# Optimization experiments

Hardware: AMD Instinct MI355X
Metric: run time of the kernel (lower is better)

## Reference

```python
import jax, jax.numpy as jnp
import numpy as np

N_HEAD = 16
EPS = 1e-6


def setup_inputs() -> dict:
    key = jax.random.key(0)
    ks = jax.random.split(key, 5)
    B, T, C = 2, 2048, 1024
    hd = C // N_HEAD
    x = jax.random.normal(ks[0], (B, T, C), dtype=jnp.float32)
    # rotary frequencies (unit-magnitude complex, decomposed into cos/sin)
    theta = 10000.0 ** (-np.arange(0, hd, 2, dtype=np.float32) / hd)  # [hd/2]
    ang = np.arange(T, dtype=np.float32)[:, None] * theta[None, :]    # [T, hd/2]
    freqs_cos = jnp.asarray(np.cos(ang))
    freqs_sin = jnp.asarray(np.sin(ang))
    w_attn = jax.random.normal(ks[1], (3 * C, C), dtype=jnp.float32) * 0.02
    w_proj = jax.random.normal(ks[2], (C, C), dtype=jnp.float32) * 0.02
    q_norm_w = jnp.ones((hd,), dtype=jnp.float32)
    k_norm_w = jnp.ones((hd,), dtype=jnp.float32)
    return {"x": x, "freqs_cos": freqs_cos, "freqs_sin": freqs_sin,
            "w_attn": w_attn, "w_proj": w_proj,
            "q_norm_w": q_norm_w, "k_norm_w": k_norm_w}


def _rmsnorm(x, w):
    # x: [..., hd]; per-last-dim RMSNorm with learned scale
    rms = jax.lax.rsqrt(jnp.mean(x * x, axis=-1, keepdims=True) + EPS)
    return x * rms * w


def _rope(x, cos, sin):
    # x: [B, T, H, hd]; cos/sin: [T, hd/2] -> broadcast [1, T, 1, hd/2]
    x2 = x.reshape(*x.shape[:-1], -1, 2)  # [B,T,H,hd/2,2]
    x0, x1 = x2[..., 0], x2[..., 1]
    c = cos[None, :, None, :]
    s = sin[None, :, None, :]
    r0 = x0 * c - x1 * s
    r1 = x0 * s + x1 * c
    return jnp.stack([r0, r1], axis=-1).reshape(x.shape)


def reference(x, freqs_cos, freqs_sin, w_attn, w_proj, q_norm_w, k_norm_w):
    B, T, C = x.shape
    H = N_HEAD
    hd = C // H
    qkv = x @ w_attn.T  # [B, T, 3C]
    q, k, v = jnp.split(qkv, 3, axis=-1)
    q = q.reshape(B, T, H, hd)
    k = k.reshape(B, T, H, hd)
    v = v.reshape(B, T, H, hd)
    q = _rmsnorm(q, q_norm_w)
    k = _rmsnorm(k, k_norm_w)
    q = _rope(q, freqs_cos[:T], freqs_sin[:T])
    k = _rope(k, freqs_cos[:T], freqs_sin[:T])
    scale = 1.0 / jnp.sqrt(jnp.asarray(hd, dtype=x.dtype))
    # causal SDPA: scores [B, H, T, T]
    scores = jnp.einsum('bihd,bjhd->bhij', q, k) * scale
    causal = jnp.tril(jnp.ones((T, T), dtype=bool))
    scores = jnp.where(causal[None, None], scores, jnp.finfo(scores.dtype).min)
    p = jax.nn.softmax(scores, axis=-1)
    y = jnp.einsum('bhij,bjhd->bihd', p, v).reshape(B, T, C)
    return y @ w_proj.T
```

## Files before the change

kernel.cpp:

```cpp
#include <hip/hip_runtime.h>

typedef unsigned short u16;
typedef unsigned int u32;
typedef __bf16 bf16x8 __attribute__((ext_vector_type(8)));
typedef float f32x4 __attribute__((ext_vector_type(4)));

__device__ __forceinline__ u16 f2bf(float f) {
    union { float f; u32 u; } v;
    v.f = f;
    u32 r = v.u + 0x7fffu + ((v.u >> 16) & 1u);
    return (u16)(r >> 16);
}

__device__ __forceinline__ u32 fbits(float f) {
    union { float f; u32 u; } v; v.f = f; return v.u;
}

__device__ __forceinline__ void glds16(const void* g, void* l) {
    __builtin_amdgcn_global_load_lds(
        (__attribute__((address_space(1))) unsigned int*)(g),
        (__attribute__((address_space(3))) unsigned int*)(l), 16, 0, 0);
}

__global__ void castbf3(const float* __restrict__ a, u16* __restrict__ oa,
                        const float* __restrict__ b, u16* __restrict__ ob,
                        const float* __restrict__ c, u16* __restrict__ oc) {
    int blk = blockIdx.x;
    if (blk < 4096) {
        int i = blk * 256 + threadIdx.x;
        float4 v = ((const float4*)a)[i];
        ushort4 o;
        o.x = f2bf(v.x); o.y = f2bf(v.y); o.z = f2bf(v.z); o.w = f2bf(v.w);
        ((ushort4*)oa)[i] = o;
    } else if (blk < 7168) {
        int i = (blk - 4096) * 256 + threadIdx.x;
        int n = i >> 8, c4 = i & 255;
        int np;
        if (n < 2048) {
            int part = n >> 10, rem = n & 1023;
            int h = rem >> 6, d = rem & 63;
            int nd = (d >> 1) + ((d & 1) << 5);
            np = part * 1024 + h * 64 + nd;
        } else np = n;
        float4 v = ((const float4*)b)[i];
        ushort4 o;
        o.x = f2bf(v.x); o.y = f2bf(v.y); o.z = f2bf(v.z); o.w = f2bf(v.w);
        ((ushort4*)ob)[np * 256 + c4] = o;
    } else {
        int i = (blk - 7168) * 256 + threadIdx.x;
        float4 v = ((const float4*)c)[i];
        ushort4 o;
        o.x = f2bf(v.x); o.y = f2bf(v.y); o.z = f2bf(v.z); o.w = f2bf(v.w);
        ((ushort4*)oc)[i] = o;
    }
}

__global__ __launch_bounds__(256) void gemm_qkv(
    const u16* __restrict__ A, const u16* __restrict__ B,
    const float* __restrict__ fcos, const float* __restrict__ fsin,
    const float* __restrict__ qw, const float* __restrict__ kw,
    u16* __restrict__ q, u16* __restrict__ k, u16* __restrict__ vt)
{
    __shared__ alignas(16) u16 As[128 * 32];
    __shared__ alignas(16) u16 Bs[128 * 32];
    __shared__ alignas(16) u16 Es[2 * 128 * 64];
    const int tid = threadIdx.x;
    const int lane = tid & 63;
    const int wave = tid >> 6;
    const int bm = blockIdx.y * 128, bn = blockIdx.x * 128;
    const int wm = (wave >> 1) * 64, wn = (wave & 1) * 64;
    const int ln = lane & 15, quad = lane >> 4;
    const int K = 1024;

    f32x4 acc[4][4] = {};

    const int srow = tid >> 2;
    const int scol = (tid & 3) * 8;
    const u16* gA = A + (size_t)(bm + srow) * K + scol;
    const u16* gB = B + (size_t)(bn + srow) * K + scol;
    u16* lA = &As[wave * 512];
    u16* lB = &Bs[wave * 512];

    for (int k0 = 0; k0 < K; k0 += 32) {
        glds16(gA + k0, lA);
        glds16(gA + (size_t)64 * K + k0, lA + 2048);
        glds16(gB + k0, lB);
        glds16(gB + (size_t)64 * K + k0, lB + 2048);
        __builtin_amdgcn_s_waitcnt(0);
        __syncthreads();

        bf16x8 af[4], bfr[4];
#pragma unroll
        for (int i = 0; i < 4; ++i)
            af[i] = *(const bf16x8*)&As[(wm + i * 16 + ln) * 32 + quad * 8];
#pragma unroll
        for (int j = 0; j < 4; ++j)
            bfr[j] = *(const bf16x8*)&Bs[(wn + j * 16 + ln) * 32 + quad * 8];
#pragma unroll
        for (int i = 0; i < 4; ++i)
#pragma unroll
            for (int j = 0; j < 4; ++j)
                acc[i][j] = __builtin_amdgcn_mfma_f32_16x16x32_bf16(af[i], bfr[j], acc[i][j], 0, 0, 0);
        __syncthreads();
    }

    const int part = bn >> 10;
    const int headw = wave & 1;
    const int h0 = (bn & 1023) >> 6;
    const float SC = 0.18033688011112042f;

    if (part == 2) {
#pragma unroll
        for (int i = 0; i < 4; ++i)
#pragma unroll
            for (int r = 0; r < 4; ++r) {
                int tloc = wm + i * 16 + quad * 4 + r;
#pragma unroll
                for (int j = 0; j < 4; ++j) {
                    int d = j * 16 + ln;
                    Es[headw * 8192 + d * 128 + (tloc ^ (ln << 3))] = f2bf(acc[i][j][r]);
                }
            }
        __syncthreads();
        const int b = bm >> 11, tbase = bm & 2047;
#pragma unroll
        for (int c = 0; c < 8; ++c) {
            int cid = c * 256 + tid;
            int tc = cid & 15, d = (cid >> 4) & 63, hd = cid >> 10;
            uint4 v = *(const uint4*)&Es[hd * 8192 + d * 128 + ((tc ^ (d & 15)) << 3)];
            size_t dst = ((size_t)((b * 16 + h0 + hd) * 64 + d)) * 2048
                       + tbase + ((tc >> 3) << 6) + (((tc & 7) ^ (d & 7)) << 3);
            *(uint4*)&vt[dst] = v;
        }
        return;
    }

    const float* nw = (part == 0) ? qw : kw;
    float wv[4];
#pragma unroll
    for (int j = 0; j < 4; ++j) {
        int nd = j * 16 + ln;
        int od = ((nd & 31) << 1) | (nd >> 5);
        wv[j] = nw[od];
    }

#pragma unroll
    for (int i = 0; i < 4; ++i) {
#pragma unroll
        for (int r = 0; r < 4; ++r) {
            int tloc = wm + i * 16 + quad * 4 + r;
            int t = (bm + tloc) & 2047;

            float v0 = acc[i][0][r], v1 = acc[i][1][r];
            float v2 = acc[i][2][r], v3 = acc[i][3][r];
            float ss = v0 * v0 + v1 * v1 + v2 * v2 + v3 * v3;
            ss += __shfl_xor(ss, 1);
            ss += __shfl_xor(ss, 2);
            ss += __shfl_xor(ss, 4);
            ss += __shfl_xor(ss, 8);
            float g = rsqrtf(ss * (1.0f / 64.0f) + 1e-6f);
            if (part == 0) g *= SC;

            float x0a = v0 * g * wv[0], x0b = v1 * g * wv[1];
            float x1a = v2 * g * wv[2], x1b = v3 * g * wv[3];
            float c0 = fcos[t * 32 + ln],      s0 = fsin[t * 32 + ln];
            float c1 = fcos[t * 32 + 16 + ln], s1 = fsin[t * 32 + 16 + ln];
            float o0 = x0a * c0 - x1a * s0;
            float o2 = x0a * s0 + x1a * c0;
            float o1 = x0b * c1 - x1b * s1;
            float o3 = x0b * s1 + x1b * c1;

            u16* e = &Es[headw * 8192 + tloc * 64 + ln];
            e[((0 ^ quad) << 4)] = f2bf(o0);
            e[((1 ^ quad) << 4)] = f2bf(o1);
            e[((2 ^ quad) << 4)] = f2bf(o2);
            e[((3 ^ quad) << 4)] = f2bf(o3);
        }
    }
    __syncthreads();
#pragma unroll
    for (int c = 0; c < 8; ++c) {
        int cid = c * 256 + tid;
        int dc = cid & 7, tloc = (cid >> 3) & 127, hd = cid >> 10;
        int q2 = (tloc >> 2) & 3;
        int sq = (dc >> 1) ^ q2;
        uint4 v = *(const uint4*)&Es[hd * 8192 + tloc * 64 + sq * 16 + (dc & 1) * 8];
        int gm = bm + tloc;
        int b = gm >> 11, t = gm & 2047;
        size_t rb = ((size_t)((b * 16 + h0 + hd) * 2048 + t)) * 64;
        if (part == 0) *(uint4*)&q[rb + dc * 8] = v;
        else           *(uint4*)&k[rb + ((dc ^ (t & 7)) << 3)] = v;
    }
}

__global__ __launch_bounds__(256) void gemm64(
    const u16* __restrict__ A, const u16* __restrict__ B,
    float* __restrict__ C, int M, int N, int K)
{
    __shared__ alignas(16) u16 As[64 * 32];
    __shared__ alignas(16) u16 Bs[128 * 32];
    const int tid = threadIdx.x;
    const int lane = tid & 63;
    const int wave = tid >> 6;
    const int bm = blockIdx.y * 64, bn = blockIdx.x * 128;
    const int wm = (wave >> 1) * 32, wn = (wave & 1) * 64;
    const int ln = lane & 15, quad = lane >> 4;

    f32x4 acc[2][4] = {};

    const int srow = tid >> 2;
    const int scol = (tid & 3) * 8;
    const u16* gA = A + (size_t)(bm + (srow & 63)) * K + scol;
    const u16* gB = B + (size_t)(bn + srow) * K + scol;
    u16* lA = &As[wave * 512];
    u16* lB = &Bs[wave * 512];

    for (int k0 = 0; k0 < K; k0 += 32) {
        glds16(gA + k0, lA);
        glds16(gB + k0, lB);
        glds16(gB + (size_t)64 * K + k0, lB + 2048);
        __builtin_amdgcn_s_waitcnt(0);
        __syncthreads();

        bf16x8 af[2], bfr[4];
#pragma unroll
        for (int i = 0; i < 2; ++i)
            af[i] = *(const bf16x8*)&As[(wm + i * 16 + ln) * 32 + quad * 8];
#pragma unroll
        for (int j = 0; j < 4; ++j)
            bfr[j] = *(const bf16x8*)&Bs[(wn + j * 16 + ln) * 32 + quad * 8];
#pragma unroll
        for (int i = 0; i < 2; ++i)
#pragma unroll
            for (int j = 0; j < 4; ++j)
                acc[i][j] = __builtin_amdgcn_mfma_f32_16x16x32_bf16(af[i], bfr[j], acc[i][j], 0, 0, 0);
        __syncthreads();
    }

#pragma unroll
    for (int i = 0; i < 2; ++i) {
#pragma unroll
        for (int r = 0; r < 4; ++r) {
            int gm = bm + wm + i * 16 + quad * 4 + r;
            float* Crow = C + (size_t)gm * N + bn + wn + ln;
#pragma unroll
            for (int j = 0; j < 4; ++j)
                Crow[j * 16] = acc[i][j][r];
        }
    }
}

__global__ __launch_bounds__(256) void attn_kernel(
    const u16* __restrict__ Q, const u16* __restrict__ K,
    const u16* __restrict__ VT, u16* __restrict__ Y)
{
    __shared__ alignas(16) u16 Ks[2][64 * 64];
    __shared__ alignas(16) u16 Vs[2][64 * 64];
    __shared__ alignas(16) u16 Ps[4][16 * 80];

    const int tid = threadIdx.x;
    const int lane = tid & 63;
    const int wave = tid >> 6;
    const int ln = lane & 15, quad = lane >> 4;
    const int pi = blockIdx.x;
    const int bh = blockIdx.y;
    const int qaIdx = pi, qbIdx = 31 - pi;
    const int qA = qaIdx * 64, qB = qbIdx * 64;
    const size_t base = (size_t)bh * 2048 * 64;
    const u16* Kg = K + base;
    const u16* Vg = VT + base;

    const int qrowA = qA + wave * 16 + ln;
    bf16x8 qfA0 = *(const bf16x8*)&Q[base + (size_t)qrowA * 64 + quad * 8];
    bf16x8 qfA1 = *(const bf16x8*)&Q[base + (size_t)qrowA * 64 + 32 + quad * 8];
    const int qrowB = qB + wave * 16 + ln;
    bf16x8 qfB0 = *(const bf16x8*)&Q[base + (size_t)qrowB * 64 + quad * 8];
    bf16x8 qfB1 = *(const bf16x8*)&Q[base + (size_t)qrowB * 64 + 32 + quad * 8];

    f32x4 oA[4] = {}, oB[4] = {};
    float lA = 0.0f, lB = 0.0f;
    const int nstages = qbIdx + 1;
    const int sw = ln & 7;

    const int srow = wave * 16 + (lane >> 3);
    const int scol = (lane & 7) * 8;

    auto process = [&](const bf16x8& qf0, const bf16x8& qf1, float& l,
                       f32x4* o, const u16* ksb, const u16* vsb, bool domask,
                       int jb, int qb0) {
        f32x4 st[4];
#pragma unroll
        for (int ct = 0; ct < 4; ++ct) {
            bf16x8 kf0 = *(const bf16x8*)&ksb[(ct * 16 + ln) * 64 + ((0 + quad) ^ sw) * 8];
            bf16x8 kf1 = *(const bf16x8*)&ksb[(ct * 16 + ln) * 64 + ((4 + quad) ^ sw) * 8];
            f32x4 z = {};
            z = __builtin_amdgcn_mfma_f32_16x16x32_bf16(kf0, qf0, z, 0, 0, 0);
            st[ct] = __builtin_amdgcn_mfma_f32_16x16x32_bf16(kf1, qf1, z, 0, 0, 0);
        }
        if (domask) {
            const int qg = qb0 + wave * 16 + ln;
#pragma unroll
            for (int ct = 0; ct < 4; ++ct)
#pragma unroll
                for (int r = 0; r < 4; ++r) {
                    int kvg = jb + ct * 16 + quad * 4 + r;
                    if (kvg > qg) st[ct][r] = -1e30f;
                }
        }

        float sum = 0.0f;
#pragma unroll
        for (int ct = 0; ct < 4; ++ct) {
            float e0 = exp2f(st[ct][0]);
            float e1 = exp2f(st[ct][1]);
            float e2 = exp2f(st[ct][2]);
            float e3 = exp2f(st[ct][3]);
            sum += (e0 + e1) + (e2 + e3);
            uint2 pk;
            pk.x = __builtin_amdgcn_perm(fbits(e1), fbits(e0), 0x07060302u);
            pk.y = __builtin_amdgcn_perm(fbits(e3), fbits(e2), 0x07060302u);
            *(uint2*)&Ps[wave][ln * 80 + ct * 16 + quad * 4] = pk;
        }
        sum += __shfl_xor(sum, 16);
        sum += __shfl_xor(sum, 32);
        l += sum;

        __builtin_amdgcn_s_waitcnt(0xC07F);
        bf16x8 pf0 = *(const bf16x8*)&Ps[wave][ln * 80 + quad * 8];
        bf16x8 pf1 = *(const bf16x8*)&Ps[wave][ln * 80 + 32 + quad * 8];

#pragma unroll
        for (int dt = 0; dt < 4; ++dt) {
            bf16x8 vf0 = *(const bf16x8*)&vsb[(dt * 16 + ln) * 64 + ((0 + quad) ^ sw) * 8];
            bf16x8 vf1 = *(const bf16x8*)&vsb[(dt * 16 + ln) * 64 + ((4 + quad) ^ sw) * 8];
            o[dt] = __builtin_amdgcn_mfma_f32_16x16x32_bf16(pf0, vf0, o[dt], 0, 0, 0);
            o[dt] = __builtin_amdgcn_mfma_f32_16x16x32_bf16(pf1, vf1, o[dt], 0, 0, 0);
        }
    };

    glds16(&Kg[(size_t)(0 + srow) * 64 + scol],       &Ks[0][wave * 1024]);
    glds16(&Kg[(size_t)(0 + srow + 8) * 64 + scol],   &Ks[0][wave * 1024 + 512]);
    glds16(&Vg[(size_t)srow * 2048 + 0 + scol],       &Vs[0][wave * 1024]);
    glds16(&Vg[(size_t)(srow + 8) * 2048 + 0 + scol], &Vs[0][wave * 1024 + 512]);

    for (int jt = 0; jt < nstages; ++jt) {
        const int jb = jt * 64;
        const int jbn = (jt + 1 < nstages) ? (jt + 1) * 64 : 0;
        const int nb = (jt + 1) & 1;
        glds16(&Kg[(size_t)(jbn + srow) * 64 + scol],       &Ks[nb][wave * 1024]);
        glds16(&Kg[(size_t)(jbn + srow + 8) * 64 + scol],   &Ks[nb][wave * 1024 + 512]);
        glds16(&Vg[(size_t)srow * 2048 + jbn + scol],       &Vs[nb][wave * 1024]);
        glds16(&Vg[(size_t)(srow + 8) * 2048 + jbn + scol], &Vs[nb][wave * 1024 + 512]);

        asm volatile("s_waitcnt vmcnt(4)\n\ts_barrier" ::: "memory");

        const u16* ksb = &Ks[jt & 1][0];
        const u16* vsb = &Vs[jt & 1][0];

        if (jt <= qaIdx)
            process(qfA0, qfA1, lA, oA, ksb, vsb, jt == qaIdx, jb, qA);
        process(qfB0, qfB1, lB, oB, ksb, vsb, jt == qbIdx, jb, qB);

        asm volatile("s_waitcnt lgkmcnt(0)\n\ts_barrier" ::: "memory");
    }

    const int b = bh >> 4, h = bh & 15;
#pragma unroll
    for (int r = 0; r < 4; ++r) {
        float lra = __shfl(lA, (lane & 48) + quad * 4 + r);
        float invA = 1.0f / lra;
        int gqA = qA + wave * 16 + quad * 4 + r;
        size_t ybA = ((size_t)(b * 2048 + gqA)) * 1024 + h * 64 + ln;
        float lrb = __shfl(lB, (lane & 48) + quad * 4 + r);
        float invB = 1.0f / lrb;
        int gqB = qB + wave * 16 + quad * 4 + r;
        size_t ybB = ((size_t)(b * 2048 + gqB)) * 1024 + h * 64 + ln;
#pragma unroll
        for (int dt = 0; dt < 4; ++dt) {
            Y[ybA + dt * 16] = f2bf(oA[dt][r] * invA);
            Y[ybB + dt * 16] = f2bf(oB[dt][r] * invB);
        }
    }
}

extern "C" void kernel_launch(void* const* d_in, const int* in_sizes, int n_in,
                              void* d_out, int out_size, void* d_ws, size_t ws_size,
                              hipStream_t stream) {
    const float* x      = (const float*)d_in[0];
    const float* fcos   = (const float*)d_in[1];
    const float* fsin   = (const float*)d_in[2];
    const float* w_attn = (const float*)d_in[3];
    const float* w_proj = (const float*)d_in[4];
    const float* qw     = (const float*)d_in[5];
    const float* kw     = (const float*)d_in[6];
    float* out = (float*)d_out;

    char* ws = (char*)d_ws;
    u16* xb  = (u16*)(ws + 0);
    u16* wab = (u16*)(ws + 8388608);
    u16* wpb = (u16*)(ws + 14680064);
    u16* yb  = (u16*)(ws + 16777216);
    u16* qb  = (u16*)(ws + 25165824);
    u16* kb  = (u16*)(ws + 33554432);
    u16* vtb = (u16*)(ws + 41943040);

    castbf3<<<8192, 256, 0, stream>>>(x, xb, w_attn, wab, w_proj, wpb);

    gemm_qkv<<<dim3(24, 32), 256, 0, stream>>>(xb, wab, fcos, fsin, qw, kw, qb, kb, vtb);

    attn_kernel<<<dim3(16, 32), 256, 0, stream>>>(qb, kb, vtb, yb);

    gemm64<<<dim3(8, 64), 256, 0, stream>>>(yb, wpb, out, 4096, 1024, 1024);
}
```

Measured before the change: 212.2 us.

## Interleave paired query-tile attention stages and pack cos/sin and V stores

```diff
diff --git a/kernel.cpp b/kernel.cpp
--- a/kernel.cpp
+++ b/kernel.cpp
@@ -22,9 +22,13 @@
         (__attribute__((address_space(3))) unsigned int*)(l), 16, 0, 0);
 }
 
+#define MFMA __builtin_amdgcn_mfma_f32_16x16x32_bf16
+
 __global__ void castbf3(const float* __restrict__ a, u16* __restrict__ oa,
                         const float* __restrict__ b, u16* __restrict__ ob,
-                        const float* __restrict__ c, u16* __restrict__ oc) {
+                        const float* __restrict__ c, u16* __restrict__ oc,
+                        const float* __restrict__ fcos, const float* __restrict__ fsin,
+                        float2* __restrict__ csb) {
     int blk = blockIdx.x;
     if (blk < 4096) {
         int i = blk * 256 + threadIdx.x;
@@ -46,18 +50,21 @@
         ushort4 o;
         o.x = f2bf(v.x); o.y = f2bf(v.y); o.z = f2bf(v.z); o.w = f2bf(v.w);
         ((ushort4*)ob)[np * 256 + c4] = o;
-    } else {
+    } else if (blk < 8192) {
         int i = (blk - 7168) * 256 + threadIdx.x;
         float4 v = ((const float4*)c)[i];
         ushort4 o;
         o.x = f2bf(v.x); o.y = f2bf(v.y); o.z = f2bf(v.z); o.w = f2bf(v.w);
         ((ushort4*)oc)[i] = o;
+    } else {
+        int i = (blk - 8192) * 256 + threadIdx.x;
+        csb[i] = make_float2(fcos[i], fsin[i]);
     }
 }
 
 __global__ __launch_bounds__(256) void gemm_qkv(
     const u16* __restrict__ A, const u16* __restrict__ B,
-    const float* __restrict__ fcos, const float* __restrict__ fsin,
+    const float2* __restrict__ csb,
     const float* __restrict__ qw, const float* __restrict__ kw,
     u16* __restrict__ q, u16* __restrict__ k, u16* __restrict__ vt)
 {
@@ -100,7 +107,7 @@
         for (int i = 0; i < 4; ++i)
 #pragma unroll
             for (int j = 0; j < 4; ++j)
-                acc[i][j] = __builtin_amdgcn_mfma_f32_16x16x32_bf16(af[i], bfr[j], acc[i][j], 0, 0, 0);
+                acc[i][j] = MFMA(af[i], bfr[j], acc[i][j], 0, 0, 0);
         __syncthreads();
     }
 
@@ -111,16 +118,17 @@
 
     if (part == 2) {
 #pragma unroll
-        for (int i = 0; i < 4; ++i)
-#pragma unroll
-            for (int r = 0; r < 4; ++r) {
-                int tloc = wm + i * 16 + quad * 4 + r;
-#pragma unroll
-                for (int j = 0; j < 4; ++j) {
-                    int d = j * 16 + ln;
-                    Es[headw * 8192 + d * 128 + (tloc ^ (ln << 3))] = f2bf(acc[i][j][r]);
-                }
+        for (int i = 0; i < 4; ++i) {
+            int tlb = wm + i * 16 + quad * 4;
+#pragma unroll
+            for (int j = 0; j < 4; ++j) {
+                int d = j * 16 + ln;
+                uint2 pk;
+                pk.x = __builtin_amdgcn_perm(fbits(acc[i][j][1]), fbits(acc[i][j][0]), 0x07060302u);
+                pk.y = __builtin_amdgcn_perm(fbits(acc[i][j][3]), fbits(acc[i][j][2]), 0x07060302u);
+                *(uint2*)&Es[headw * 8192 + d * 128 + (tlb ^ (ln << 3))] = pk;
             }
+        }
         __syncthreads();
         const int b = bm >> 11, tbase = bm & 2047;
 #pragma unroll
@@ -163,12 +171,12 @@
 
             float x0a = v0 * g * wv[0], x0b = v1 * g * wv[1];
             float x1a = v2 * g * wv[2], x1b = v3 * g * wv[3];
-            float c0 = fcos[t * 32 + ln],      s0 = fsin[t * 32 + ln];
-            float c1 = fcos[t * 32 + 16 + ln], s1 = fsin[t * 32 + 16 + ln];
-            float o0 = x0a * c0 - x1a * s0;
-            float o2 = x0a * s0 + x1a * c0;
-            float o1 = x0b * c1 - x1b * s1;
-            float o3 = x0b * s1 + x1b * c1;
+            float2 cs0 = csb[t * 32 + ln];
+            float2 cs1 = csb[t * 32 + 16 + ln];
+            float o0 = x0a * cs0.x - x1a * cs0.y;
+            float o2 = x0a * cs0.y + x1a * cs0.x;
+            float o1 = x0b * cs1.x - x1b * cs1.y;
+            float o3 = x0b * cs1.y + x1b * cs1.x;
 
             u16* e = &Es[headw * 8192 + tloc * 64 + ln];
             e[((0 ^ quad) << 4)] = f2bf(o0);
@@ -233,7 +241,7 @@
         for (int i = 0; i < 2; ++i)
 #pragma unroll
             for (int j = 0; j < 4; ++j)
-                acc[i][j] = __builtin_amdgcn_mfma_f32_16x16x32_bf16(af[i], bfr[j], acc[i][j], 0, 0, 0);
+                acc[i][j] = MFMA(af[i], bfr[j], acc[i][j], 0, 0, 0);
         __syncthreads();
     }
 
@@ -246,6 +254,98 @@
 #pragma unroll
             for (int j = 0; j < 4; ++j)
                 Crow[j * 16] = acc[i][j][r];
+        }
+    }
+}
+
+template <bool DUAL>
+__device__ __forceinline__ void attn_stage(
+    int ln, int quad, int sw,
+    const u16* __restrict__ ksb, const u16* __restrict__ vsb,
+    u16* __restrict__ PsA, u16* __restrict__ PsB,
+    const bf16x8& qfA0, const bf16x8& qfA1,
+    const bf16x8& qfB0, const bf16x8& qfB1,
+    f32x4* oA, f32x4* oB, float& lA, float& lB,
+    bool maskA, bool maskB, int jb, int qA, int qB)
+{
+    f32x4 stA[4], stB[4];
+#pragma unroll
+    for (int ct = 0; ct < 4; ++ct) {
+        bf16x8 kf0 = *(const bf16x8*)&ksb[(ct * 16 + ln) * 64 + ((0 + quad) ^ sw) * 8];
+        bf16x8 kf1 = *(const bf16x8*)&ksb[(ct * 16 + ln) * 64 + ((4 + quad) ^ sw) * 8];
+        f32x4 z = {};
+        z = MFMA(kf0, qfB0, z, 0, 0, 0);
+        stB[ct] = MFMA(kf1, qfB1, z, 0, 0, 0);
+        if (DUAL) {
+            f32x4 za = {};
+            za = MFMA(kf0, qfA0, za, 0, 0, 0);
+            stA[ct] = MFMA(kf1, qfA1, za, 0, 0, 0);
+        }
+    }
+    if (maskB) {
+        const int qg = qB + ln;
+#pragma unroll
+        for (int ct = 0; ct < 4; ++ct)
+#pragma unroll
+            for (int r = 0; r < 4; ++r)
+                if (jb + ct * 16 + quad * 4 + r > qg) stB[ct][r] = -1e30f;
+    }
+    if (DUAL && maskA) {
+        const int qg = qA + ln;
+#pragma unroll
+        for (int ct = 0; ct < 4; ++ct)
+#pragma unroll
+            for (int r = 0; r < 4; ++r)
+                if (jb + ct * 16 + quad * 4 + r > qg) stA[ct][r] = -1e30f;
+    }
+
+    float sumB = 0.0f, sumA = 0.0f;
+#pragma unroll
+    for (int ct = 0; ct < 4; ++ct) {
+        float b0 = exp2f(stB[ct][0]), b1 = exp2f(stB[ct][1]);
+        float b2 = exp2f(stB[ct][2]), b3 = exp2f(stB[ct][3]);
+        sumB += (b0 + b1) + (b2 + b3);
+        uint2 pk;
+        pk.x = __builtin_amdgcn_perm(fbits(b1), fbits(b0), 0x07060302u);
+        pk.y = __builtin_amdgcn_perm(fbits(b3), fbits(b2), 0x07060302u);
+        *(uint2*)&PsB[ln * 80 + ct * 16 + quad * 4] = pk;
+        if (DUAL) {
+            float a0 = exp2f(stA[ct][0]), a1 = exp2f(stA[ct][1]);
+            float a2 = exp2f(stA[ct][2]), a3 = exp2f(stA[ct][3]);
+            sumA += (a0 + a1) + (a2 + a3);
+            uint2 pa;
+            pa.x = __builtin_amdgcn_perm(fbits(a1), fbits(a0), 0x07060302u);
+            pa.y = __builtin_amdgcn_perm(fbits(a3), fbits(a2), 0x07060302u);
+            *(uint2*)&PsA[ln * 80 + ct * 16 + quad * 4] = pa;
+        }
+    }
+    sumB += __shfl_xor(sumB, 16);
+    sumB += __shfl_xor(sumB, 32);
+    lB += sumB;
+    if (DUAL) {
+        sumA += __shfl_xor(sumA, 16);
+        sumA += __shfl_xor(sumA, 32);
+        lA += sumA;
+    }
+
+    __builtin_amdgcn_s_waitcnt(0xC07F);
+    bf16x8 pfB0 = *(const bf16x8*)&PsB[ln * 80 + quad * 8];
+    bf16x8 pfB1 = *(const bf16x8*)&PsB[ln * 80 + 32 + quad * 8];
+    bf16x8 pfA0, pfA1;
+    if (DUAL) {
+        pfA0 = *(const bf16x8*)&PsA[ln * 80 + quad * 8];
+        pfA1 = *(const bf16x8*)&PsA[ln * 80 + 32 + quad * 8];
+    }
+
+#pragma unroll
+    for (int dt = 0; dt < 4; ++dt) {
+        bf16x8 vf0 = *(const bf16x8*)&vsb[(dt * 16 + ln) * 64 + ((0 + quad) ^ sw) * 8];
+        bf16x8 vf1 = *(const bf16x8*)&vsb[(dt * 16 + ln) * 64 + ((4 + quad) ^ sw) * 8];
+        oB[dt] = MFMA(pfB0, vf0, oB[dt], 0, 0, 0);
+        oB[dt] = MFMA(pfB1, vf1, oB[dt], 0, 0, 0);
+        if (DUAL) {
+            oA[dt] = MFMA(pfA0, vf0, oA[dt], 0, 0, 0);
+            oA[dt] = MFMA(pfA1, vf1, oA[dt], 0, 0, 0);
         }
     }
 }
@@ -256,7 +356,8 @@
 {
     __shared__ alignas(16) u16 Ks[2][64 * 64];
     __shared__ alignas(16) u16 Vs[2][64 * 64];
-    __shared__ alignas(16) u16 Ps[4][16 * 80];
+    __shared__ alignas(16) u16 PsA[4][16 * 80];
+    __shared__ alignas(16) u16 PsB[4][16 * 80];
 
     const int tid = threadIdx.x;
     const int lane = tid & 63;
@@ -285,82 +386,34 @@
     const int srow = wave * 16 + (lane >> 3);
     const int scol = (lane & 7) * 8;
 
-    auto process = [&](const bf16x8& qf0, const bf16x8& qf1, float& l,
-                       f32x4* o, const u16* ksb, const u16* vsb, bool domask,
-                       int jb, int qb0) {
-        f32x4 st[4];
-#pragma unroll
-        for (int ct = 0; ct < 4; ++ct) {
-            bf16x8 kf0 = *(const bf16x8*)&ksb[(ct * 16 + ln) * 64 + ((0 + quad) ^ sw) * 8];
-            bf16x8 kf1 = *(const bf16x8*)&ksb[(ct * 16 + ln) * 64 + ((4 + quad) ^ sw) * 8];
-            f32x4 z = {};
-            z = __builtin_amdgcn_mfma_f32_16x16x32_bf16(kf0, qf0, z, 0, 0, 0);
-            st[ct] = __builtin_amdgcn_mfma_f32_16x16x32_bf16(kf1, qf1, z, 0, 0, 0);
-        }
-        if (domask) {
-            const int qg = qb0 + wave * 16 + ln;
-#pragma unroll
-            for (int ct = 0; ct < 4; ++ct)
-#pragma unroll
-                for (int r = 0; r < 4; ++r) {
-                    int kvg = jb + ct * 16 + quad * 4 + r;
-                    if (kvg > qg) st[ct][r] = -1e30f;
-                }
-        }
-
-        float sum = 0.0f;
-#pragma unroll
-        for (int ct = 0; ct < 4; ++ct) {
-            float e0 = exp2f(st[ct][0]);
-            float e1 = exp2f(st[ct][1]);
-            float e2 = exp2f(st[ct][2]);
-            float e3 = exp2f(st[ct][3]);
-            sum += (e0 + e1) + (e2 + e3);
-            uint2 pk;
-            pk.x = __builtin_amdgcn_perm(fbits(e1), fbits(e0), 0x07060302u);
-            pk.y = __builtin_amdgcn_perm(fbits(e3), fbits(e2), 0x07060302u);
-            *(uint2*)&Ps[wave][ln * 80 + ct * 16 + quad * 4] = pk;
-        }
-        sum += __shfl_xor(sum, 16);
-        sum += __shfl_xor(sum, 32);
-        l += sum;
-
-        __builtin_amdgcn_s_waitcnt(0xC07F);
-        bf16x8 pf0 = *(const bf16x8*)&Ps[wave][ln * 80 + quad * 8];
-        bf16x8 pf1 = *(const bf16x8*)&Ps[wave][ln * 80 + 32 + quad * 8];
-
-#pragma unroll
-        for (int dt = 0; dt < 4; ++dt) {
-            bf16x8 vf0 = *(const bf16x8*)&vsb[(dt * 16 + ln) * 64 + ((0 + quad) ^ sw) * 8];
-            bf16x8 vf1 = *(const bf16x8*)&vsb[(dt * 16 + ln) * 64 + ((4 + quad) ^ sw) * 8];
-            o[dt] = __builtin_amdgcn_mfma_f32_16x16x32_bf16(pf0, vf0, o[dt], 0, 0, 0);
-            o[dt] = __builtin_amdgcn_mfma_f32_16x16x32_bf16(pf1, vf1, o[dt], 0, 0, 0);
-        }
-    };
-
-    glds16(&Kg[(size_t)(0 + srow) * 64 + scol],       &Ks[0][wave * 1024]);
-    glds16(&Kg[(size_t)(0 + srow + 8) * 64 + scol],   &Ks[0][wave * 1024 + 512]);
-    glds16(&Vg[(size_t)srow * 2048 + 0 + scol],       &Vs[0][wave * 1024]);
-    glds16(&Vg[(size_t)(srow + 8) * 2048 + 0 + scol], &Vs[0][wave * 1024 + 512]);
-
-    for (int jt = 0; jt < nstages; ++jt) {
-        const int jb = jt * 64;
-        const int jbn = (jt + 1 < nstages) ? (jt + 1) * 64 : 0;
-        const int nb = (jt + 1) & 1;
+    auto prefetch = [&](int jbn, int nb) {
         glds16(&Kg[(size_t)(jbn + srow) * 64 + scol],       &Ks[nb][wave * 1024]);
         glds16(&Kg[(size_t)(jbn + srow + 8) * 64 + scol],   &Ks[nb][wave * 1024 + 512]);
         glds16(&Vg[(size_t)srow * 2048 + jbn + scol],       &Vs[nb][wave * 1024]);
         glds16(&Vg[(size_t)(srow + 8) * 2048 + jbn + scol], &Vs[nb][wave * 1024 + 512]);
-
+    };
+
+    prefetch(0, 0);
+
+    int jt = 0;
+    for (; jt <= qaIdx; ++jt) {
+        const int jbn = (jt + 1 < nstages) ? (jt + 1) * 64 : 0;
+        prefetch(jbn, (jt + 1) & 1);
         asm volatile("s_waitcnt vmcnt(4)\n\ts_barrier" ::: "memory");
-
-        const u16* ksb = &Ks[jt & 1][0];
-        const u16* vsb = &Vs[jt & 1][0];
-
-        if (jt <= qaIdx)
-            process(qfA0, qfA1, lA, oA, ksb, vsb, jt == qaIdx, jb, qA);
-        process(qfB0, qfB1, lB, oB, ksb, vsb, jt == qbIdx, jb, qB);
-
+        attn_stage<true>(ln, quad, sw, &Ks[jt & 1][0], &Vs[jt & 1][0],
+                         &PsA[wave][0], &PsB[wave][0],
+                         qfA0, qfA1, qfB0, qfB1, oA, oB, lA, lB,
+                         jt == qaIdx, false, jt * 64, qA + wave * 16, qB + wave * 16);
+        asm volatile("s_waitcnt lgkmcnt(0)\n\ts_barrier" ::: "memory");
+    }
+    for (; jt < nstages; ++jt) {
+        const int jbn = (jt + 1 < nstages) ? (jt + 1) * 64 : 0;
+        prefetch(jbn, (jt + 1) & 1);
+        asm volatile("s_waitcnt vmcnt(4)\n\ts_barrier" ::: "memory");
+        attn_stage<false>(ln, quad, sw, &Ks[jt & 1][0], &Vs[jt & 1][0],
+                          &PsA[wave][0], &PsB[wave][0],
+                          qfA0, qfA1, qfB0, qfB1, oA, oB, lA, lB,
+                          false, jt == qbIdx, jt * 64, qA + wave * 16, qB + wave * 16);
         asm volatile("s_waitcnt lgkmcnt(0)\n\ts_barrier" ::: "memory");
     }
 
@@ -396,17 +449,18 @@
     float* out = (float*)d_out;
 
     char* ws = (char*)d_ws;
-    u16* xb  = (u16*)(ws + 0);
-    u16* wab = (u16*)(ws + 8388608);
-    u16* wpb = (u16*)(ws + 14680064);
-    u16* yb  = (u16*)(ws + 16777216);
-    u16* qb  = (u16*)(ws + 25165824);
-    u16* kb  = (u16*)(ws + 33554432);
-    u16* vtb = (u16*)(ws + 41943040);
-
-    castbf3<<<8192, 256, 0, stream>>>(x, xb, w_attn, wab, w_proj, wpb);
-
-    gemm_qkv<<<dim3(24, 32), 256, 0, stream>>>(xb, wab, fcos, fsin, qw, kw, qb, kb, vtb);
+    u16*    xb  = (u16*)(ws + 0);
+    u16*    wab = (u16*)(ws + 8388608);
+    u16*    wpb = (u16*)(ws + 14680064);
+    u16*    yb  = (u16*)(ws + 16777216);
+    u16*    qb  = (u16*)(ws + 25165824);
+    u16*    kb  = (u16*)(ws + 33554432);
+    u16*    vtb = (u16*)(ws + 41943040);
+    float2* csb = (float2*)(ws + 50331648);
+
+    castbf3<<<8448, 256, 0, stream>>>(x, xb, w_attn, wab, w_proj, wpb, fcos, fsin, csb);
+
+    gemm_qkv<<<dim3(24, 32), 256, 0, stream>>>(xb, wab, csb, qw, kw, qb, kb, vtb);
 
     attn_kernel<<<dim3(16, 32), 256, 0, stream>>>(qb, kb, vtb, yb);
 
```

Measured after the change: 209.0 us. Within noise of the previous version (-1.5%).

## Split attention query pair across 8 waves and store Q transposed

Applied to the files above, without the earlier changes.

```diff
diff --git a/kernel.cpp b/kernel.cpp
--- a/kernel.cpp
+++ b/kernel.cpp
@@ -22,9 +22,13 @@
         (__attribute__((address_space(3))) unsigned int*)(l), 16, 0, 0);
 }
 
+#define MFMA __builtin_amdgcn_mfma_f32_16x16x32_bf16
+
 __global__ void castbf3(const float* __restrict__ a, u16* __restrict__ oa,
                         const float* __restrict__ b, u16* __restrict__ ob,
-                        const float* __restrict__ c, u16* __restrict__ oc) {
+                        const float* __restrict__ c, u16* __restrict__ oc,
+                        const float* __restrict__ fcos, const float* __restrict__ fsin,
+                        float2* __restrict__ csb) {
     int blk = blockIdx.x;
     if (blk < 4096) {
         int i = blk * 256 + threadIdx.x;
@@ -46,18 +50,21 @@
         ushort4 o;
         o.x = f2bf(v.x); o.y = f2bf(v.y); o.z = f2bf(v.z); o.w = f2bf(v.w);
         ((ushort4*)ob)[np * 256 + c4] = o;
-    } else {
+    } else if (blk < 8192) {
         int i = (blk - 7168) * 256 + threadIdx.x;
         float4 v = ((const float4*)c)[i];
         ushort4 o;
         o.x = f2bf(v.x); o.y = f2bf(v.y); o.z = f2bf(v.z); o.w = f2bf(v.w);
         ((ushort4*)oc)[i] = o;
+    } else {
+        int i = (blk - 8192) * 256 + threadIdx.x;
+        csb[i] = make_float2(fcos[i], fsin[i]);
     }
 }
 
 __global__ __launch_bounds__(256) void gemm_qkv(
     const u16* __restrict__ A, const u16* __restrict__ B,
-    const float* __restrict__ fcos, const float* __restrict__ fsin,
+    const float2* __restrict__ csb,
     const float* __restrict__ qw, const float* __restrict__ kw,
     u16* __restrict__ q, u16* __restrict__ k, u16* __restrict__ vt)
 {
@@ -100,7 +107,7 @@
         for (int i = 0; i < 4; ++i)
 #pragma unroll
             for (int j = 0; j < 4; ++j)
-                acc[i][j] = __builtin_amdgcn_mfma_f32_16x16x32_bf16(af[i], bfr[j], acc[i][j], 0, 0, 0);
+                acc[i][j] = MFMA(af[i], bfr[j], acc[i][j], 0, 0, 0);
         __syncthreads();
     }
 
@@ -108,21 +115,22 @@
     const int headw = wave & 1;
     const int h0 = (bn & 1023) >> 6;
     const float SC = 0.18033688011112042f;
+    const int b = bm >> 11, tbase = bm & 2047;
 
     if (part == 2) {
 #pragma unroll
-        for (int i = 0; i < 4; ++i)
-#pragma unroll
-            for (int r = 0; r < 4; ++r) {
-                int tloc = wm + i * 16 + quad * 4 + r;
-#pragma unroll
-                for (int j = 0; j < 4; ++j) {
-                    int d = j * 16 + ln;
-                    Es[headw * 8192 + d * 128 + (tloc ^ (ln << 3))] = f2bf(acc[i][j][r]);
-                }
-            }
-        __syncthreads();
-        const int b = bm >> 11, tbase = bm & 2047;
+        for (int i = 0; i < 4; ++i) {
+            int tlb = wm + i * 16 + quad * 4;
+#pragma unroll
+            for (int j = 0; j < 4; ++j) {
+                int d = j * 16 + ln;
+                uint2 pk;
+                pk.x = __builtin_amdgcn_perm(fbits(acc[i][j][1]), fbits(acc[i][j][0]), 0x07060302u);
+                pk.y = __builtin_amdgcn_perm(fbits(acc[i][j][3]), fbits(acc[i][j][2]), 0x07060302u);
+                *(uint2*)&Es[headw * 8192 + d * 128 + (tlb ^ (ln << 3))] = pk;
+            }
+        }
+        __syncthreads();
 #pragma unroll
         for (int c = 0; c < 8; ++c) {
             int cid = c * 256 + tid;
@@ -142,6 +150,52 @@
         int nd = j * 16 + ln;
         int od = ((nd & 31) << 1) | (nd >> 5);
         wv[j] = nw[od];
+    }
+
+    if (part == 0) {
+#pragma unroll
+        for (int i = 0; i < 4; ++i) {
+            float oj[4][4];
+#pragma unroll
+            for (int r = 0; r < 4; ++r) {
+                int tloc = wm + i * 16 + quad * 4 + r;
+                int t = (bm + tloc) & 2047;
+                float v0 = acc[i][0][r], v1 = acc[i][1][r];
+                float v2 = acc[i][2][r], v3 = acc[i][3][r];
+                float ss = v0 * v0 + v1 * v1 + v2 * v2 + v3 * v3;
+                ss += __shfl_xor(ss, 1);
+                ss += __shfl_xor(ss, 2);
+                ss += __shfl_xor(ss, 4);
+                ss += __shfl_xor(ss, 8);
+                float g = rsqrtf(ss * (1.0f / 64.0f) + 1e-6f) * SC;
+                float x0a = v0 * g * wv[0], x0b = v1 * g * wv[1];
+                float x1a = v2 * g * wv[2], x1b = v3 * g * wv[3];
+                float2 cs0 = csb[t * 32 + ln];
+                float2 cs1 = csb[t * 32 + 16 + ln];
+                oj[0][r] = x0a * cs0.x - x1a * cs0.y;
+                oj[2][r] = x0a * cs0.y + x1a * cs0.x;
+                oj[1][r] = x0b * cs1.x - x1b * cs1.y;
+                oj[3][r] = x0b * cs1.y + x1b * cs1.x;
+            }
+            int tlb = wm + i * 16 + quad * 4;
+#pragma unroll
+            for (int j = 0; j < 4; ++j) {
+                uint2 pk;
+                pk.x = __builtin_amdgcn_perm(fbits(oj[j][1]), fbits(oj[j][0]), 0x07060302u);
+                pk.y = __builtin_amdgcn_perm(fbits(oj[j][3]), fbits(oj[j][2]), 0x07060302u);
+                *(uint2*)&Es[headw * 8192 + (j * 16 + ln) * 128 + (tlb ^ (ln << 3))] = pk;
+            }
+        }
+        __syncthreads();
+#pragma unroll
+        for (int c = 0; c < 8; ++c) {
+            int cid = c * 256 + tid;
+            int tc = cid & 15, d = (cid >> 4) & 63, hd = cid >> 10;
+            uint4 v = *(const uint4*)&Es[hd * 8192 + d * 128 + ((tc ^ (d & 15)) << 3)];
+            size_t dst = ((size_t)((b * 16 + h0 + hd) * 64 + d)) * 2048 + tbase + tc * 8;
+            *(uint4*)&q[dst] = v;
+        }
+        return;
     }
 
 #pragma unroll
@@ -159,16 +213,15 @@
             ss += __shfl_xor(ss, 4);
             ss += __shfl_xor(ss, 8);
             float g = rsqrtf(ss * (1.0f / 64.0f) + 1e-6f);
-            if (part == 0) g *= SC;
 
             float x0a = v0 * g * wv[0], x0b = v1 * g * wv[1];
             float x1a = v2 * g * wv[2], x1b = v3 * g * wv[3];
-            float c0 = fcos[t * 32 + ln],      s0 = fsin[t * 32 + ln];
-            float c1 = fcos[t * 32 + 16 + ln], s1 = fsin[t * 32 + 16 + ln];
-            float o0 = x0a * c0 - x1a * s0;
-            float o2 = x0a * s0 + x1a * c0;
-            float o1 = x0b * c1 - x1b * s1;
-            float o3 = x0b * s1 + x1b * c1;
+            float2 cs0 = csb[t * 32 + ln];
+            float2 cs1 = csb[t * 32 + 16 + ln];
+            float o0 = x0a * cs0.x - x1a * cs0.y;
+            float o2 = x0a * cs0.y + x1a * cs0.x;
+            float o1 = x0b * cs1.x - x1b * cs1.y;
+            float o3 = x0b * cs1.y + x1b * cs1.x;
 
             u16* e = &Es[headw * 8192 + tloc * 64 + ln];
             e[((0 ^ quad) << 4)] = f2bf(o0);
@@ -186,10 +239,9 @@
         int sq = (dc >> 1) ^ q2;
         uint4 v = *(const uint4*)&Es[hd * 8192 + tloc * 64 + sq * 16 + (dc & 1) * 8];
         int gm = bm + tloc;
-        int b = gm >> 11, t = gm & 2047;
-        size_t rb = ((size_t)((b * 16 + h0 + hd) * 2048 + t)) * 64;
-        if (part == 0) *(uint4*)&q[rb + dc * 8] = v;
-        else           *(uint4*)&k[rb + ((dc ^ (t & 7)) << 3)] = v;
+        int bb = gm >> 11, t = gm & 2047;
+        size_t rb = ((size_t)((bb * 16 + h0 + hd) * 2048 + t)) * 64;
+        *(uint4*)&k[rb + ((dc ^ (t & 7)) << 3)] = v;
     }
 }
 
@@ -233,7 +285,7 @@
         for (int i = 0; i < 2; ++i)
 #pragma unroll
             for (int j = 0; j < 4; ++j)
-                acc[i][j] = __builtin_amdgcn_mfma_f32_16x16x32_bf16(af[i], bfr[j], acc[i][j], 0, 0, 0);
+                acc[i][j] = MFMA(af[i], bfr[j], acc[i][j], 0, 0, 0);
         __syncthreads();
     }
 
@@ -250,13 +302,13 @@
     }
 }
 
-__global__ __launch_bounds__(256) void attn_kernel(
+__global__ __launch_bounds__(512) void attn_kernel(
     const u16* __restrict__ Q, const u16* __restrict__ K,
     const u16* __restrict__ VT, u16* __restrict__ Y)
 {
     __shared__ alignas(16) u16 Ks[2][64 * 64];
     __shared__ alignas(16) u16 Vs[2][64 * 64];
-    __shared__ alignas(16) u16 Ps[4][16 * 80];
+    __shared__ alignas(16) u16 Ps[8][16 * 80];
 
     const int tid = threadIdx.x;
     const int lane = tid & 63;
@@ -265,121 +317,104 @@
     const int pi = blockIdx.x;
     const int bh = blockIdx.y;
     const int qaIdx = pi, qbIdx = 31 - pi;
-    const int qA = qaIdx * 64, qB = qbIdx * 64;
+    const bool isB = wave >= 4;
+    const int qidx = isB ? qbIdx : qaIdx;
+    const int myq = qidx * 64 + (wave & 3) * 16;
     const size_t base = (size_t)bh * 2048 * 64;
     const u16* Kg = K + base;
     const u16* Vg = VT + base;
-
-    const int qrowA = qA + wave * 16 + ln;
-    bf16x8 qfA0 = *(const bf16x8*)&Q[base + (size_t)qrowA * 64 + quad * 8];
-    bf16x8 qfA1 = *(const bf16x8*)&Q[base + (size_t)qrowA * 64 + 32 + quad * 8];
-    const int qrowB = qB + wave * 16 + ln;
-    bf16x8 qfB0 = *(const bf16x8*)&Q[base + (size_t)qrowB * 64 + quad * 8];
-    bf16x8 qfB1 = *(const bf16x8*)&Q[base + (size_t)qrowB * 64 + 32 + quad * 8];
-
-    f32x4 oA[4] = {}, oB[4] = {};
-    float lA = 0.0f, lB = 0.0f;
+    const __bf16* Qg = (const __bf16*)(Q + base);
+
+    const int qt = myq + ln;
+    bf16x8 qf0, qf1;
+#pragma unroll
+    for (int j = 0; j < 8; ++j) {
+        qf0[j] = Qg[(size_t)(quad * 8 + j) * 2048 + qt];
+        qf1[j] = Qg[(size_t)(32 + quad * 8 + j) * 2048 + qt];
+    }
+
+    f32x4 o[4] = {};
+    float l = 0.0f;
     const int nstages = qbIdx + 1;
     const int sw = ln & 7;
-
-    const int srow = wave * 16 + (lane >> 3);
+    const int srow = wave * 8 + (lane >> 3);
     const int scol = (lane & 7) * 8;
-
-    auto process = [&](const bf16x8& qf0, const bf16x8& qf1, float& l,
-                       f32x4* o, const u16* ksb, const u16* vsb, bool domask,
-                       int jb, int qb0) {
-        f32x4 st[4];
-#pragma unroll
-        for (int ct = 0; ct < 4; ++ct) {
-            bf16x8 kf0 = *(const bf16x8*)&ksb[(ct * 16 + ln) * 64 + ((0 + quad) ^ sw) * 8];
-            bf16x8 kf1 = *(const bf16x8*)&ksb[(ct * 16 + ln) * 64 + ((4 + quad) ^ sw) * 8];
-            f32x4 z = {};
-            z = __builtin_amdgcn_mfma_f32_16x16x32_bf16(kf0, qf0, z, 0, 0, 0);
-            st[ct] = __builtin_amdgcn_mfma_f32_16x16x32_bf16(kf1, qf1, z, 0, 0, 0);
-        }
-        if (domask) {
-            const int qg = qb0 + wave * 16 + ln;
-#pragma unroll
-            for (int ct = 0; ct < 4; ++ct)
-#pragma unroll
-                for (int r = 0; r < 4; ++r) {
-                    int kvg = jb + ct * 16 + quad * 4 + r;
-                    if (kvg > qg) st[ct][r] = -1e30f;
-                }
-        }
-
-        float sum = 0.0f;
-#pragma unroll
-        for (int ct = 0; ct < 4; ++ct) {
-            float e0 = exp2f(st[ct][0]);
-            float e1 = exp2f(st[ct][1]);
-            float e2 = exp2f(st[ct][2]);
-            float e3 = exp2f(st[ct][3]);
-            sum += (e0 + e1) + (e2 + e3);
-            uint2 pk;
-            pk.x = __builtin_amdgcn_perm(fbits(e1), fbits(e0), 0x07060302u);
-            pk.y = __builtin_amdgcn_perm(fbits(e3), fbits(e2), 0x07060302u);
-            *(uint2*)&Ps[wave][ln * 80 + ct * 16 + quad * 4] = pk;
-        }
-        sum += __shfl_xor(sum, 16);
-        sum += __shfl_xor(sum, 32);
-        l += sum;
-
-        __builtin_amdgcn_s_waitcnt(0xC07F);
-        bf16x8 pf0 = *(const bf16x8*)&Ps[wave][ln * 80 + quad * 8];
-        bf16x8 pf1 = *(const bf16x8*)&Ps[wave][ln * 80 + 32 + quad * 8];
-
-#pragma unroll
-        for (int dt = 0; dt < 4; ++dt) {
-            bf16x8 vf0 = *(const bf16x8*)&vsb[(dt * 16 + ln) * 64 + ((0 + quad) ^ sw) * 8];
-            bf16x8 vf1 = *(const bf16x8*)&vsb[(dt * 16 + ln) * 64 + ((4 + quad) ^ sw) * 8];
-            o[dt] = __builtin_amdgcn_mfma_f32_16x16x32_bf16(pf0, vf0, o[dt], 0, 0, 0);
-            o[dt] = __builtin_amdgcn_mfma_f32_16x16x32_bf16(pf1, vf1, o[dt], 0, 0, 0);
-        }
+    u16* Psw = &Ps[wave][0];
+
+    auto prefetch = [&](int jb, int nb) {
+        glds16(&Kg[(size_t)(jb + srow) * 64 + scol], &Ks[nb][wave * 512]);
+        glds16(&Vg[(size_t)srow * 2048 + jb + scol], &Vs[nb][wave * 512]);
     };
-
-    glds16(&Kg[(size_t)(0 + srow) * 64 + scol],       &Ks[0][wave * 1024]);
-    glds16(&Kg[(size_t)(0 + srow + 8) * 64 + scol],   &Ks[0][wave * 1024 + 512]);
-    glds16(&Vg[(size_t)srow * 2048 + 0 + scol],       &Vs[0][wave * 1024]);
-    glds16(&Vg[(size_t)(srow + 8) * 2048 + 0 + scol], &Vs[0][wave * 1024 + 512]);
+    prefetch(0, 0);
 
     for (int jt = 0; jt < nstages; ++jt) {
-        const int jb = jt * 64;
         const int jbn = (jt + 1 < nstages) ? (jt + 1) * 64 : 0;
-        const int nb = (jt + 1) & 1;
-        glds16(&Kg[(size_t)(jbn + srow) * 64 + scol],       &Ks[nb][wave * 1024]);
-        glds16(&Kg[(size_t)(jbn + srow + 8) * 64 + scol],   &Ks[nb][wave * 1024 + 512]);
-        glds16(&Vg[(size_t)srow * 2048 + jbn + scol],       &Vs[nb][wave * 1024]);
-        glds16(&Vg[(size_t)(srow + 8) * 2048 + jbn + scol], &Vs[nb][wave * 1024 + 512]);
-
-        asm volatile("s_waitcnt vmcnt(4)\n\ts_barrier" ::: "memory");
+        prefetch(jbn, (jt + 1) & 1);
+        asm volatile("s_waitcnt vmcnt(2)\n\ts_barrier" ::: "memory");
 
         const u16* ksb = &Ks[jt & 1][0];
         const u16* vsb = &Vs[jt & 1][0];
 
-        if (jt <= qaIdx)
-            process(qfA0, qfA1, lA, oA, ksb, vsb, jt == qaIdx, jb, qA);
-        process(qfB0, qfB1, lB, oB, ksb, vsb, jt == qbIdx, jb, qB);
-
+        if (isB || jt <= qaIdx) {
+            f32x4 st[4];
+#pragma unroll
+            for (int ct = 0; ct < 4; ++ct) {
+                bf16x8 kf0 = *(const bf16x8*)&ksb[(ct * 16 + ln) * 64 + ((0 + quad) ^ sw) * 8];
+                bf16x8 kf1 = *(const bf16x8*)&ksb[(ct * 16 + ln) * 64 + ((4 + quad) ^ sw) * 8];
+                f32x4 z = {};
+                z = MFMA(kf0, qf0, z, 0, 0, 0);
+                st[ct] = MFMA(kf1, qf1, z, 0, 0, 0);
+            }
+            if (jt == qidx) {
+                const int qg = myq + ln;
+                const int jb = jt * 64;
+#pragma unroll
+                for (int ct = 0; ct < 4; ++ct)
+#pragma unroll
+                    for (int r = 0; r < 4; ++r)
+                        if (jb + ct * 16 + quad * 4 + r > qg) st[ct][r] = -1e30f;
+            }
+
+            float sum = 0.0f;
+#pragma unroll
+            for (int ct = 0; ct < 4; ++ct) {
+                float e0 = exp2f(st[ct][0]), e1 = exp2f(st[ct][1]);
+                float e2 = exp2f(st[ct][2]), e3 = exp2f(st[ct][3]);
+                sum += (e0 + e1) + (e2 + e3);
+                uint2 pk;
+                pk.x = __builtin_amdgcn_perm(fbits(e1), fbits(e0), 0x07060302u);
+                pk.y = __builtin_amdgcn_perm(fbits(e3), fbits(e2), 0x07060302u);
+                *(uint2*)&Psw[ln * 80 + ct * 16 + quad * 4] = pk;
+            }
+            sum += __shfl_xor(sum, 16);
+            sum += __shfl_xor(sum, 32);
+            l += sum;
+
+            __builtin_amdgcn_s_waitcnt(0xC07F);
+            bf16x8 pf0 = *(const bf16x8*)&Psw[ln * 80 + quad * 8];
+            bf16x8 pf1 = *(const bf16x8*)&Psw[ln * 80 + 32 + quad * 8];
+
+#pragma unroll
+            for (int dt = 0; dt < 4; ++dt) {
+                bf16x8 vf0 = *(const bf16x8*)&vsb[(dt * 16 + ln) * 64 + ((0 + quad) ^ sw) * 8];
+                bf16x8 vf1 = *(const bf16x8*)&vsb[(dt * 16 + ln) * 64 + ((4 + quad) ^ sw) * 8];
+                o[dt] = MFMA(pf0, vf0, o[dt], 0, 0, 0);
+                o[dt] = MFMA(pf1, vf1, o[dt], 0, 0, 0);
+            }
+        }
         asm volatile("s_waitcnt lgkmcnt(0)\n\ts_barrier" ::: "memory");
     }
 
     const int b = bh >> 4, h = bh & 15;
 #pragma unroll
     for (int r = 0; r < 4; ++r) {
-        float lra = __shfl(lA, (lane & 48) + quad * 4 + r);
-        float invA = 1.0f / lra;
-        int gqA = qA + wave * 16 + quad * 4 + r;
-        size_t ybA = ((size_t)(b * 2048 + gqA)) * 1024 + h * 64 + ln;
-        float lrb = __shfl(lB, (lane & 48) + quad * 4 + r);
-        float invB = 1.0f / lrb;
-        int gqB = qB + wave * 16 + quad * 4 + r;
-        size_t ybB = ((size_t)(b * 2048 + gqB)) * 1024 + h * 64 + ln;
-#pragma unroll
-        for (int dt = 0; dt < 4; ++dt) {
-            Y[ybA + dt * 16] = f2bf(oA[dt][r] * invA);
-            Y[ybB + dt * 16] = f2bf(oB[dt][r] * invB);
-        }
+        float lr = __shfl(l, (lane & 48) + quad * 4 + r);
+        float inv = 1.0f / lr;
+        int gq = myq + quad * 4 + r;
+        size_t yb = ((size_t)(b * 2048 + gq)) * 1024 + h * 64 + ln;
+#pragma unroll
+        for (int dt = 0; dt < 4; ++dt)
+            Y[yb + dt * 16] = f2bf(o[dt][r] * inv);
     }
 }
 
@@ -396,19 +431,20 @@
     float* out = (float*)d_out;
 
     char* ws = (char*)d_ws;
-    u16* xb  = (u16*)(ws + 0);
-    u16* wab = (u16*)(ws + 8388608);
-    u16* wpb = (u16*)(ws + 14680064);
-    u16* yb  = (u16*)(ws + 16777216);
-    u16* qb  = (u16*)(ws + 25165824);
-    u16* kb  = (u16*)(ws + 33554432);
-    u16* vtb = (u16*)(ws + 41943040);
-
-    castbf3<<<8192, 256, 0, stream>>>(x, xb, w_attn, wab, w_proj, wpb);
-
-    gemm_qkv<<<dim3(24, 32), 256, 0, stream>>>(xb, wab, fcos, fsin, qw, kw, qb, kb, vtb);
-
-    attn_kernel<<<dim3(16, 32), 256, 0, stream>>>(qb, kb, vtb, yb);
+    u16*    xb  = (u16*)(ws + 0);
+    u16*    yb  = (u16*)(ws + 0);
+    u16*    wab = (u16*)(ws + 8388608);
+    u16*    wpb = (u16*)(ws + 14680064);
+    u16*    qb  = (u16*)(ws + 16777216);
+    u16*    kb  = (u16*)(ws + 25165824);
+    u16*    vtb = (u16*)(ws + 33554432);
+    float2* csb = (float2*)(ws + 41943040);
+
+    castbf3<<<8448, 256, 0, stream>>>(x, xb, w_attn, wab, w_proj, wpb, fcos, fsin, csb);
+
+    gemm_qkv<<<dim3(24, 32), 256, 0, stream>>>(xb, wab, csb, qw, kw, qb, kb, vtb);
+
+    attn_kernel<<<dim3(16, 32), 512, 0, stream>>>(qb, kb, vtb, yb);
 
     gemm64<<<dim3(8, 64), 256, 0, stream>>>(yb, wpb, out, 4096, 1024, 1024);
 }
```

New measurement: 206.7 us. -2.6%, faster.
